# Kernel tuning notes

Hardware: AMD Instinct MI355X
Metric: run time of the kernel (lower is better)

Reference implementation:

```python
import jax, jax.numpy as jnp
import numpy as np

N = 1_000_000          # number of RoIs
C = 4                  # num_class (foreground classes)
IMG_H, IMG_W = 1080.0, 1920.0
BBOX_MEAN = jnp.array([0.0, 0.0, 0.0, 0.0], jnp.float32)
BBOX_STD = jnp.array([0.1, 0.1, 0.2, 0.2], jnp.float32)
THR_OBJ = 0.2          # threshold_objectness
THR_CLS = 0.1          # thresholds[0]
MIN_W, MIN_H = 6.0, 6.0
MAX_CAND = 300         # nms max_candidate_n
OVERLAP = 0.5          # nms overlap_ratio
TOP_N = 100            # nms top_n


def setup_inputs() -> dict:
    key = jax.random.key(0)
    k1, k2, k3, k4, k5 = jax.random.split(key, 5)
    logits = jax.random.normal(k1, (N, C + 1), jnp.float32) * 2.0
    cls_score_softmax = jax.nn.softmax(logits, axis=-1)          # rows sum to 1, like softmax output
    bbox_pred = jax.random.normal(k2, (N, 4 * (C + 1)), jnp.float32) * 0.5
    x1 = jax.random.uniform(k3, (N,), jnp.float32, 0.0, IMG_W * 0.8)
    y1 = jax.random.uniform(k4, (N,), jnp.float32, 0.0, IMG_H * 0.8)
    wh = jax.random.uniform(k5, (N, 2), jnp.float32, 8.0, 200.0)
    rois = jnp.stack([jnp.zeros((N,), jnp.float32), x1, y1, x1 + wh[:, 0], y1 + wh[:, 1]], axis=1)
    im_info = jnp.array([IMG_H, IMG_W], jnp.float32)
    return {"cls_score_softmax": cls_score_softmax, "bbox_pred": bbox_pred, "rois": rois, "im_info": im_info}


def _pairwise_iou(b):
    # torchvision box_iou convention: area = (x2-x1)*(y2-y1), no +1
    lt = jnp.maximum(b[:, None, :2], b[None, :, :2])
    rb = jnp.minimum(b[:, None, 2:], b[None, :, 2:])
    wh = jnp.clip(rb - lt, 0.0)
    inter = wh[..., 0] * wh[..., 1]
    area = (b[:, 2] - b[:, 0]) * (b[:, 3] - b[:, 1])
    return inter / (area[:, None] + area[None, :] - inter)


def _forward(cls_score_softmax, bbox_pred, rois, im_info):
    h_img, w_img = im_info[0], im_info[1]
    # denormalize deltas and decode against rois (bbox_transform_inv_rcnn)
    deltas = (bbox_pred.reshape(-1, 4) * BBOX_STD + BBOX_MEAN).reshape(-1, C + 1, 4)
    bx = rois[:, 1:]
    w = bx[:, 2] - bx[:, 0] + 1.0
    h = bx[:, 3] - bx[:, 1] + 1.0
    cx = bx[:, 0] + 0.5 * (w - 1.0)
    cy = bx[:, 1] + 0.5 * (h - 1.0)
    pcx = deltas[:, :, 0] * w[:, None] + cx[:, None]
    pcy = deltas[:, :, 1] * h[:, None] + cy[:, None]
    pw = jnp.exp(deltas[:, :, 2]) * w[:, None]
    ph = jnp.exp(deltas[:, :, 3]) * h[:, None]
    pred = jnp.stack([pcx - 0.5 * (pw - 1.0), pcy - 0.5 * (ph - 1.0),
                      pcx + 0.5 * (pw - 1.0), pcy + 0.5 * (ph - 1.0)], axis=-1)  # [N, C+1, 4]
    # refine_out_of_map_bbox: clip to image
    pred = jnp.stack([jnp.clip(pred[..., 0], 0.0, w_img - 1.0),
                      jnp.clip(pred[..., 1], 0.0, h_img - 1.0),
                      jnp.clip(pred[..., 2], 0.0, w_img - 1.0),
                      jnp.clip(pred[..., 3], 0.0, h_img - 1.0)], axis=-1)
    # objectness + class-score filters (masked instead of compacted: jit-friendly)
    mask_obj = (1.0 - cls_score_softmax[:, 0]) >= THR_OBJ
    maxes = jnp.max(cls_score_softmax[:, 1:], axis=1)
    argmaxes = jnp.argmax(cls_score_softmax[:, 1:], axis=1) + 1
    mask_cls = maxes > THR_CLS
    # select the box of the argmax class per row
    box = jnp.take_along_axis(pred, argmaxes[:, None, None], axis=1)[:, 0, :]  # [N, 4]
    bw = box[:, 2] - box[:, 0] + 1.0
    bh = box[:, 3] - box[:, 1] + 1.0
    mask_size = (bw >= MIN_W) | (bh >= MIN_H)  # HEIGHT_OR_WIDTH
    valid = mask_obj & mask_cls & mask_size
    # top-k candidates by max class prob (invalid rows pushed below any real score)
    cand_scores = jnp.where(valid, maxes, -1.0)
    top_vals, top_idx = jax.lax.top_k(cand_scores, MAX_CAND)   # sorted descending
    cand_boxes = box[top_idx]                                   # [M, 4]
    cand_probs = cls_score_softmax[top_idx]                     # [M, C+1]
    cand_valid = top_vals > -0.5
    # greedy NMS over the (score-sorted) candidates
    iou = _pairwise_iou(cand_boxes)
    idx = jnp.arange(MAX_CAND)

    def body(i, keep):
        sup = keep[i] & (iou[i] > OVERLAP) & (idx > i)
        return keep & ~sup

    keep = jax.lax.fori_loop(0, MAX_CAND, body, cand_valid)
    # compact kept rows into the first TOP_N slots (drop-row scatter trick)
    order = jnp.cumsum(keep.astype(jnp.int32)) - 1
    slot = jnp.where(keep & (order < TOP_N), order, TOP_N)
    rows = jnp.concatenate([jnp.zeros((MAX_CAND, 1), cand_boxes.dtype), cand_boxes, cand_probs], axis=1)
    out = jnp.zeros((TOP_N + 1, rows.shape[1]), rows.dtype).at[slot].set(rows)[:TOP_N]
    return out  # [TOP_N, 1 + 4 + (C+1)] = [100, 10], zero-padded past the kept count


def reference(cls_score_softmax, bbox_pred, rois, im_info):
    return _forward(cls_score_softmax, bbox_pred, rois, im_info)
```

## Files before the change

### kernel.cpp

```cpp
#include <hip/hip_runtime.h>
#include <math.h>

#define NBINS 4096
#define CAP   4096
#define MAXC  300
#define MAXCP 320
#define TOPN  100

__device__ __forceinline__ void decode4(float x1, float y1, float x2, float y2,
                                        float4 d4, float Wimg, float Himg,
                                        float& bx1, float& by1, float& bx2, float& by2)
{
    float w  = x2 - x1 + 1.0f;
    float h  = y2 - y1 + 1.0f;
    float cx = x1 + 0.5f*(w - 1.0f);
    float cy = y1 + 0.5f*(h - 1.0f);
    float d0 = d4.x*0.1f, d1 = d4.y*0.1f, d2 = d4.z*0.2f, d3 = d4.w*0.2f;
    float pcx = d0*w + cx;
    float pcy = d1*h + cy;
    float pw  = expf(d2)*w;
    float ph  = expf(d3)*h;
    bx1 = fminf(fmaxf(pcx - 0.5f*(pw-1.0f), 0.0f), Wimg-1.0f);
    by1 = fminf(fmaxf(pcy - 0.5f*(ph-1.0f), 0.0f), Himg-1.0f);
    bx2 = fminf(fmaxf(pcx + 0.5f*(pw-1.0f), 0.0f), Wimg-1.0f);
    by2 = fminf(fmaxf(pcy + 0.5f*(ph-1.0f), 0.0f), Himg-1.0f);
}

__global__ __launch_bounds__(256)
void rcnn_pass1(const float4* __restrict__ cls4, const float4* __restrict__ bbox4,
                const float4* __restrict__ rois4, const float* __restrict__ iminfo,
                float4* __restrict__ scores4,
                unsigned int* __restrict__ hist, unsigned int* __restrict__ counter, int Ng)
{
    if (blockIdx.x == 0) {
        for (int k = threadIdx.x; k < NBINS; k += 256) hist[k] = 0u;
        if (threadIdx.x == 0) *counter = 0u;
    }

    int g = blockIdx.x * blockDim.x + threadIdx.x;
    if (g >= Ng) return;

    float c[20], q[20];
    #pragma unroll
    for (int v = 0; v < 5; v++) {
        float4 cv = cls4[5*g + v];
        c[4*v] = cv.x; c[4*v+1] = cv.y; c[4*v+2] = cv.z; c[4*v+3] = cv.w;
        float4 rv = rois4[5*g + v];
        q[4*v] = rv.x; q[4*v+1] = rv.y; q[4*v+2] = rv.z; q[4*v+3] = rv.w;
    }
    float Himg = iminfo[0], Wimg = iminfo[1];

    float s[4];
    #pragma unroll
    for (int j = 0; j < 4; j++) {
        float p0 = c[5*j], p1 = c[5*j+1], p2 = c[5*j+2], p3 = c[5*j+3], p4 = c[5*j+4];
        float m = p1; int a = 1;
        if (p2 > m) { m = p2; a = 2; }
        if (p3 > m) { m = p3; a = 3; }
        if (p4 > m) { m = p4; a = 4; }
        float sc = -1.0f;
        if (((1.0f - p0) >= 0.2f) && (m > 0.1f)) {
            float4 d4 = bbox4[20*g + 5*j + a];
            float bx1, by1, bx2, by2;
            decode4(q[5*j+1], q[5*j+2], q[5*j+3], q[5*j+4], d4, Wimg, Himg, bx1, by1, bx2, by2);
            float bw = bx2 - bx1 + 1.0f;
            float bh = by2 - by1 + 1.0f;
            if ((bw >= 6.0f) || (bh >= 6.0f)) sc = m;
        }
        s[j] = sc;
    }
    scores4[g] = make_float4(s[0], s[1], s[2], s[3]);
}

__global__ __launch_bounds__(1024)
void rcnn_hist(const float4* __restrict__ scores4, unsigned int* __restrict__ hist, int Ng)
{
    __shared__ unsigned int lh[NBINS];
    const int t = threadIdx.x;
    for (int k = t; k < NBINS; k += 1024) lh[k] = 0u;
    __syncthreads();

    int stride = gridDim.x * 1024;
    for (int g = blockIdx.x * 1024 + t; g < Ng; g += stride) {
        float4 s4 = scores4[g];
        float ss[4] = { s4.x, s4.y, s4.z, s4.w };
        #pragma unroll
        for (int j = 0; j < 4; j++) {
            float s = ss[j];
            if (s > -0.5f) {
                int bin = (int)(s * (float)NBINS);
                bin = bin > NBINS-1 ? NBINS-1 : bin;
                atomicAdd(&lh[bin], 1u);
            }
        }
    }
    __syncthreads();
    for (int k = t; k < NBINS; k += 1024) {
        unsigned int v = lh[k];
        if (v) atomicAdd(&hist[k], v);
    }
}

__global__ __launch_bounds__(1024)
void rcnn_pass2(const unsigned int* __restrict__ hist, int* __restrict__ taubin)
{
    __shared__ unsigned int suf[1024];
    __shared__ int g_sh;
    int t = threadIdx.x;
    unsigned int v = hist[4*t] + hist[4*t+1] + hist[4*t+2] + hist[4*t+3];
    suf[t] = v;
    __syncthreads();
    for (int d = 1; d < 1024; d <<= 1) {
        unsigned int add = (t + d < 1024) ? suf[t + d] : 0u;
        __syncthreads();
        suf[t] += add;
        __syncthreads();
    }
    if (t == 0) g_sh = -1;
    __syncthreads();
    if (suf[t] >= MAXC && (t == 1023 || suf[t+1] < MAXC)) g_sh = t;
    __syncthreads();
    if (t == 0) {
        int g = g_sh;
        int tau = 0;
        if (g >= 0) {
            unsigned int cum = (g == 1023) ? 0u : suf[g+1];
            tau = 4*g;
            for (int k = 3; k >= 0; k--) {
                cum += hist[4*g + k];
                if (cum >= MAXC) { tau = 4*g + k; break; }
            }
        }
        *taubin = tau;
    }
}

__global__ __launch_bounds__(256)
void rcnn_pass3(const float4* __restrict__ scores4, const int* __restrict__ taubin,
                float* __restrict__ cscore, int* __restrict__ cidx,
                unsigned int* __restrict__ counter, int Ng)
{
    int g = blockIdx.x * blockDim.x + threadIdx.x;
    if (g >= Ng) return;
    float4 s4 = scores4[g];
    int tau = *taubin;
    float ss[4] = { s4.x, s4.y, s4.z, s4.w };
    #pragma unroll
    for (int j = 0; j < 4; j++) {
        float s = ss[j];
        if (s > -0.5f) {
            int bin = (int)(s * (float)NBINS);
            bin = bin > NBINS-1 ? NBINS-1 : bin;
            if (bin >= tau) {
                unsigned int pos = atomicAdd(counter, 1u);
                if (pos < CAP) { cscore[pos] = s; cidx[pos] = 4*g + j; }
            }
        }
    }
}

__global__ __launch_bounds__(1024)
void rcnn_final(const float* __restrict__ cls, const float* __restrict__ bbox,
                const float* __restrict__ rois, const float* __restrict__ iminfo,
                const float* __restrict__ cscore, const int* __restrict__ cidx,
                const unsigned int* __restrict__ counter, float* __restrict__ out)
{
    __shared__ float s_s[CAP];
    __shared__ int   s_id[CAP];
    __shared__ float ts[MAXC];
    __shared__ int   tid_[MAXC];
    __shared__ float bx_[MAXCP][4];
    __shared__ float pr_[MAXC][5];
    __shared__ unsigned long long sup[MAXC][5];
    __shared__ unsigned long long maskw[5];
    __shared__ float orows[TOPN*10];
    const int t  = threadIdx.x;
    const int NT = 1024;
    int M = (int)*counter; if (M > CAP) M = CAP;

    for (int i = t; i < M; i += NT)  { s_s[i] = cscore[i]; s_id[i] = cidx[i]; }
    for (int r = t; r < MAXC; r += NT) { ts[r] = -1.0f; tid_[r] = -1; }
    for (int r = t; r < MAXCP; r += NT) { bx_[r][0]=0.0f; bx_[r][1]=0.0f; bx_[r][2]=0.0f; bx_[r][3]=0.0f; }
    if (t < 5) maskw[t] = 0ull;
    for (int k = t; k < TOPN*10; k += NT) orows[k] = 0.0f;
    __syncthreads();

    for (int i = t; i < M; i += NT) {
        float si = s_s[i]; int di = s_id[i];
        int r = 0;
        for (int j = 0; j < M; j++) {
            float sj = s_s[j];
            int   dj = s_id[j];
            r += (sj > si) || (sj == si && dj < di);
        }
        if (r < MAXC) { ts[r] = si; tid_[r] = di; }
    }
    __syncthreads();

    float Himg = iminfo[0], Wimg = iminfo[1];
    for (int r = t; r < MAXC; r += NT) {
        int i = tid_[r];
        if (i >= 0) {
            float p0 = cls[5*i], p1 = cls[5*i+1], p2 = cls[5*i+2], p3 = cls[5*i+3], p4 = cls[5*i+4];
            pr_[r][0]=p0; pr_[r][1]=p1; pr_[r][2]=p2; pr_[r][3]=p3; pr_[r][4]=p4;
            float m = p1; int a = 1;
            if (p2 > m) { m = p2; a = 2; }
            if (p3 > m) { m = p3; a = 3; }
            if (p4 > m) { m = p4; a = 4; }
            float4 d4 = ((const float4*)bbox)[5*i + a];
            float bx1, by1, bx2, by2;
            decode4(rois[5*i+1], rois[5*i+2], rois[5*i+3], rois[5*i+4], d4, Wimg, Himg, bx1, by1, bx2, by2);
            bx_[r][0]=bx1; bx_[r][1]=by1; bx_[r][2]=bx2; bx_[r][3]=by2;
            atomicOr(&maskw[r>>6], 1ull << (r & 63));
        }
    }
    __syncthreads();

    for (int task = t; task < MAXC*5; task += NT) {
        int w = task / MAXC;
        int i = task - w*MAXC;
        unsigned long long bits = 0ull;
        int j0 = w << 6;
        if (j0 + 63 > i) {
            float ax1 = bx_[i][0], ay1 = bx_[i][1], ax2 = bx_[i][2], ay2 = bx_[i][3];
            float areaA = (ax2-ax1)*(ay2-ay1);
            for (int b = 0; b < 64; b++) {
                int j = j0 + b;
                float b1 = bx_[j][0], b2 = bx_[j][1], b3 = bx_[j][2], b4 = bx_[j][3];
                float lx = fmaxf(ax1, b1), ly = fmaxf(ay1, b2);
                float rx = fminf(ax2, b3), ry = fminf(ay2, b4);
                float iw = fmaxf(rx - lx, 0.0f), ih = fmaxf(ry - ly, 0.0f);
                float inter = iw * ih;
                float areaB = (b3 - b1) * (b4 - b2);
                float iou = inter / (areaA + areaB - inter);
                bits |= (iou > 0.5f) ? (1ull << b) : 0ull;
            }
            unsigned long long jgt = (i < j0) ? ~0ull
                                  : ((i - j0) >= 63 ? 0ull : ~((1ull << (i - j0 + 1)) - 1ull));
            bits &= jgt & maskw[w];
        }
        sup[i][w] = bits;
    }
    __syncthreads();

    if (t == 0) {
        unsigned long long kw[5];
        #pragma unroll
        for (int qq = 0; qq < 5; qq++) kw[qq] = maskw[qq];
        #pragma unroll
        for (int w2 = 0; w2 < 5; w2++) {
            int nb = (w2 == 4) ? (MAXC - 4*64) : 64;
            for (int b = 0; b < nb; b++) {
                int i = (w2 << 6) + b;
                unsigned long long m = ((kw[w2] >> b) & 1ull) ? ~0ull : 0ull;
                kw[0] &= ~(sup[i][0] & m);
                kw[1] &= ~(sup[i][1] & m);
                kw[2] &= ~(sup[i][2] & m);
                kw[3] &= ~(sup[i][3] & m);
                kw[4] &= ~(sup[i][4] & m);
            }
        }
        #pragma unroll
        for (int qq = 0; qq < 5; qq++) maskw[qq] = kw[qq];
    }
    __syncthreads();

    for (int r = t; r < MAXC; r += NT) {
        if ((maskw[r>>6] >> (r & 63)) & 1ull) {
            int ord = 0;
            for (int w2 = 0; w2 < (r >> 6); w2++) ord += __popcll(maskw[w2]);
            ord += __popcll(maskw[r>>6] & ((1ull << (r & 63)) - 1ull));
            if (ord < TOPN) {
                float* row = &orows[ord*10];
                row[0] = 0.0f;
                row[1] = bx_[r][0]; row[2] = bx_[r][1]; row[3] = bx_[r][2]; row[4] = bx_[r][3];
                row[5] = pr_[r][0]; row[6] = pr_[r][1]; row[7] = pr_[r][2]; row[8] = pr_[r][3]; row[9] = pr_[r][4];
            }
        }
    }
    __syncthreads();
    for (int k = t; k < TOPN*10; k += NT) out[k] = orows[k];
}

extern "C" void kernel_launch(void* const* d_in, const int* in_sizes, int n_in,
                              void* d_out, int out_size, void* d_ws, size_t ws_size,
                              hipStream_t stream)
{
    const float* cls    = (const float*)d_in[0];
    const float* bbox   = (const float*)d_in[1];
    const float* rois   = (const float*)d_in[2];
    const float* iminfo = (const float*)d_in[3];
    int N  = in_sizes[0] / 5;
    int Ng = N / 4;

    char* ws = (char*)d_ws;
    float* scores = (float*)ws;
    size_t off = ((size_t)N * 4 + 255) & ~(size_t)255;
    unsigned int* hist    = (unsigned int*)(ws + off); off += NBINS * 4;
    int*          taubin  = (int*)(ws + off);          off += 256;
    unsigned int* counter = (unsigned int*)(ws + off); off += 256;
    float*        cscore  = (float*)(ws + off);        off += CAP * 4;
    int*          cidx    = (int*)(ws + off);          off += CAP * 4;

    int blocksG = (Ng + 255) / 256;
    rcnn_pass1<<<blocksG, 256, 0, stream>>>((const float4*)cls, (const float4*)bbox,
                                            (const float4*)rois, iminfo,
                                            (float4*)scores, hist, counter, Ng);
    rcnn_hist<<<64, 1024, 0, stream>>>((const float4*)scores, hist, Ng);
    rcnn_pass2<<<1, 1024, 0, stream>>>(hist, taubin);
    rcnn_pass3<<<blocksG, 256, 0, stream>>>((const float4*)scores, taubin,
                                            cscore, cidx, counter, Ng);
    rcnn_final<<<1, 1024, 0, stream>>>(cls, bbox, rois, iminfo,
                                       cscore, cidx, counter, (float*)d_out);
}
```

Before: 220.4 us.

## Add second-level sub-histogram to tighten top-k threshold before candidate compaction

Adds a second histogram pass over the scores falling in the threshold bin, then a kernel that picks a sub-bin threshold so that about MAXC candidates survive. The aim is fewer candidates reaching the final single-block kernel, which has less to sort and select, and fewer global atomics in pass3. The cost is two extra kernel launches and one more full read of the scores array.

```diff
diff --git a/kernel.cpp b/kernel.cpp
--- a/kernel.cpp
+++ b/kernel.cpp
@@ -6,6 +6,17 @@
 #define MAXC  300
 #define MAXCP 320
 #define TOPN  100
+
+__device__ __forceinline__ int bin_of(float s) {
+    int b = (int)(s * (float)NBINS);
+    return b > NBINS-1 ? NBINS-1 : b;
+}
+__device__ __forceinline__ int subbin_of(float s, int tau) {
+    float f = s * (float)NBINS - (float)tau;
+    int sb = (int)(f * (float)NBINS);
+    sb = sb < 0 ? 0 : (sb > NBINS-1 ? NBINS-1 : sb);
+    return sb;
+}
 
 __device__ __forceinline__ void decode4(float x1, float y1, float x2, float y2,
                                         float4 d4, float Wimg, float Himg,
@@ -30,10 +41,11 @@
 void rcnn_pass1(const float4* __restrict__ cls4, const float4* __restrict__ bbox4,
                 const float4* __restrict__ rois4, const float* __restrict__ iminfo,
                 float4* __restrict__ scores4,
-                unsigned int* __restrict__ hist, unsigned int* __restrict__ counter, int Ng)
+                unsigned int* __restrict__ hist, unsigned int* __restrict__ hist2,
+                unsigned int* __restrict__ counter, int Ng)
 {
     if (blockIdx.x == 0) {
-        for (int k = threadIdx.x; k < NBINS; k += 256) hist[k] = 0u;
+        for (int k = threadIdx.x; k < NBINS; k += 256) { hist[k] = 0u; hist2[k] = 0u; }
         if (threadIdx.x == 0) *counter = 0u;
     }
 
@@ -79,20 +91,13 @@
     const int t = threadIdx.x;
     for (int k = t; k < NBINS; k += 1024) lh[k] = 0u;
     __syncthreads();
-
     int stride = gridDim.x * 1024;
     for (int g = blockIdx.x * 1024 + t; g < Ng; g += stride) {
         float4 s4 = scores4[g];
         float ss[4] = { s4.x, s4.y, s4.z, s4.w };
         #pragma unroll
-        for (int j = 0; j < 4; j++) {
-            float s = ss[j];
-            if (s > -0.5f) {
-                int bin = (int)(s * (float)NBINS);
-                bin = bin > NBINS-1 ? NBINS-1 : bin;
-                atomicAdd(&lh[bin], 1u);
-            }
-        }
+        for (int j = 0; j < 4; j++)
+            if (ss[j] > -0.5f) atomicAdd(&lh[bin_of(ss[j])], 1u);
     }
     __syncthreads();
     for (int k = t; k < NBINS; k += 1024) {
@@ -107,8 +112,7 @@
     __shared__ unsigned int suf[1024];
     __shared__ int g_sh;
     int t = threadIdx.x;
-    unsigned int v = hist[4*t] + hist[4*t+1] + hist[4*t+2] + hist[4*t+3];
-    suf[t] = v;
+    suf[t] = hist[4*t] + hist[4*t+1] + hist[4*t+2] + hist[4*t+3];
     __syncthreads();
     for (int d = 1; d < 1024; d <<= 1) {
         unsigned int add = (t + d < 1024) ? suf[t + d] : 0u;
@@ -135,23 +139,97 @@
     }
 }
 
+__global__ __launch_bounds__(1024)
+void rcnn_hist2(const float4* __restrict__ scores4, const int* __restrict__ taubin,
+                unsigned int* __restrict__ hist2, int Ng)
+{
+    __shared__ unsigned int lh[NBINS];
+    const int t = threadIdx.x;
+    const int tau = *taubin;
+    for (int k = t; k < NBINS; k += 1024) lh[k] = 0u;
+    __syncthreads();
+    int stride = gridDim.x * 1024;
+    for (int g = blockIdx.x * 1024 + t; g < Ng; g += stride) {
+        float4 s4 = scores4[g];
+        float ss[4] = { s4.x, s4.y, s4.z, s4.w };
+        #pragma unroll
+        for (int j = 0; j < 4; j++)
+            if (ss[j] > -0.5f && bin_of(ss[j]) == tau)
+                atomicAdd(&lh[subbin_of(ss[j], tau)], 1u);
+    }
+    __syncthreads();
+    for (int k = t; k < NBINS; k += 1024) {
+        unsigned int v = lh[k];
+        if (v) atomicAdd(&hist2[k], v);
+    }
+}
+
+__global__ __launch_bounds__(1024)
+void rcnn_pass2b(const unsigned int* __restrict__ hist, const unsigned int* __restrict__ hist2,
+                 const int* __restrict__ taubin, int* __restrict__ tau2out)
+{
+    __shared__ unsigned int red[1024];
+    __shared__ unsigned int suf[1024];
+    __shared__ int g_sh;
+    __shared__ unsigned int need_sh;
+    int t = threadIdx.x;
+    int tau = *taubin;
+    unsigned int acc = 0;
+    for (int k = tau + 1 + t; k < NBINS; k += 1024) acc += hist[k];
+    red[t] = acc;
+    __syncthreads();
+    for (int d = 512; d > 0; d >>= 1) { if (t < d) red[t] += red[t + d]; __syncthreads(); }
+    if (t == 0) {
+        unsigned int C1 = red[0];
+        need_sh = (C1 >= MAXC) ? 1u : (unsigned int)(MAXC - C1);
+    }
+    __syncthreads();
+    unsigned int need = need_sh;
+    suf[t] = hist2[4*t] + hist2[4*t+1] + hist2[4*t+2] + hist2[4*t+3];
+    __syncthreads();
+    for (int d = 1; d < 1024; d <<= 1) {
+        unsigned int add = (t + d < 1024) ? suf[t + d] : 0u;
+        __syncthreads();
+        suf[t] += add;
+        __syncthreads();
+    }
+    if (t == 0) g_sh = -1;
+    __syncthreads();
+    if (suf[t] >= need && (t == 1023 || suf[t+1] < need)) g_sh = t;
+    __syncthreads();
+    if (t == 0) {
+        int g = g_sh;
+        int tau2 = 0;
+        if (g >= 0) {
+            unsigned int cum = (g == 1023) ? 0u : suf[g+1];
+            tau2 = 4*g;
+            for (int k = 3; k >= 0; k--) {
+                cum += hist2[4*g + k];
+                if (cum >= need) { tau2 = 4*g + k; break; }
+            }
+        }
+        *tau2out = tau2;
+    }
+}
+
 __global__ __launch_bounds__(256)
 void rcnn_pass3(const float4* __restrict__ scores4, const int* __restrict__ taubin,
+                const int* __restrict__ tau2bin,
                 float* __restrict__ cscore, int* __restrict__ cidx,
                 unsigned int* __restrict__ counter, int Ng)
 {
     int g = blockIdx.x * blockDim.x + threadIdx.x;
     if (g >= Ng) return;
     float4 s4 = scores4[g];
-    int tau = *taubin;
+    int tau = *taubin, tau2 = *tau2bin;
     float ss[4] = { s4.x, s4.y, s4.z, s4.w };
     #pragma unroll
     for (int j = 0; j < 4; j++) {
         float s = ss[j];
         if (s > -0.5f) {
-            int bin = (int)(s * (float)NBINS);
-            bin = bin > NBINS-1 ? NBINS-1 : bin;
-            if (bin >= tau) {
+            int bin = bin_of(s);
+            bool sel = (bin > tau) || (bin == tau && subbin_of(s, tau) >= tau2);
+            if (sel) {
                 unsigned int pos = atomicAdd(counter, 1u);
                 if (pos < CAP) { cscore[pos] = s; cidx[pos] = 4*g + j; }
             }
@@ -297,7 +375,9 @@
     float* scores = (float*)ws;
     size_t off = ((size_t)N * 4 + 255) & ~(size_t)255;
     unsigned int* hist    = (unsigned int*)(ws + off); off += NBINS * 4;
+    unsigned int* hist2   = (unsigned int*)(ws + off); off += NBINS * 4;
     int*          taubin  = (int*)(ws + off);          off += 256;
+    int*          tau2bin = (int*)(ws + off);          off += 256;
     unsigned int* counter = (unsigned int*)(ws + off); off += 256;
     float*        cscore  = (float*)(ws + off);        off += CAP * 4;
     int*          cidx    = (int*)(ws + off);          off += CAP * 4;
@@ -305,10 +385,12 @@
     int blocksG = (Ng + 255) / 256;
     rcnn_pass1<<<blocksG, 256, 0, stream>>>((const float4*)cls, (const float4*)bbox,
                                             (const float4*)rois, iminfo,
-                                            (float4*)scores, hist, counter, Ng);
+                                            (float4*)scores, hist, hist2, counter, Ng);
     rcnn_hist<<<64, 1024, 0, stream>>>((const float4*)scores, hist, Ng);
     rcnn_pass2<<<1, 1024, 0, stream>>>(hist, taubin);
-    rcnn_pass3<<<blocksG, 256, 0, stream>>>((const float4*)scores, taubin,
+    rcnn_hist2<<<64, 1024, 0, stream>>>((const float4*)scores, taubin, hist2, Ng);
+    rcnn_pass2b<<<1, 1024, 0, stream>>>(hist, hist2, taubin, tau2bin);
+    rcnn_pass3<<<blocksG, 256, 0, stream>>>((const float4*)scores, taubin, tau2bin,
                                             cscore, cidx, counter, Ng);
     rcnn_final<<<1, 1024, 0, stream>>>(cls, bbox, rois, iminfo,
                                        cscore, cidx, counter, (float*)d_out);
```

New measurement: 226.7 us. +2.9%, slower.
